# Kernel optimization log

Measured on AMD Instinct MI355X. Metric: run time of the kernel, lower is better.

Reference implementation:

```python
import jax, jax.numpy as jnp
import numpy as np
from jax import lax

GROUPS = 32
EPS = 1e-5
N_STEPS = 8   # fixed-step stand-in for adaptive implicit_adams
N_CORR = 2    # trapezoidal (Adams-Moulton) corrector iterations


def group_norm(x, gamma, beta):
    B, C, H, W = x.shape
    xg = x.reshape(B, GROUPS, C // GROUPS, H, W)
    mean = xg.mean(axis=(2, 3, 4), keepdims=True)
    var = xg.var(axis=(2, 3, 4), keepdims=True)
    xg = (xg - mean) * lax.rsqrt(var + EPS)
    return xg.reshape(B, C, H, W) * gamma[None, :, None, None] + beta[None, :, None, None]


def batch_norm1d(x, gamma, beta):  # training-mode batch stats, x: [B,C,L]
    mean = x.mean(axis=(0, 2), keepdims=True)
    var = x.var(axis=(0, 2), keepdims=True)
    return (x - mean) * lax.rsqrt(var + EPS) * gamma[None, :, None] + beta[None, :, None]


def conv1d(x, w, b):  # x [B,Cin,L], w [Cout,Cin,3], pad=1
    y = lax.conv_general_dilated(x, w, (1,), [(1, 1)], dimension_numbers=('NCH', 'OIH', 'NCH'))
    return y + b[None, :, None]


def concat_conv2d(t, x, w, b):  # x [B,C,H,W], w [C, C+1, 3,3], pad=1
    tt = jnp.full_like(x[:, :1], t)
    ttx = jnp.concatenate([tt, x], axis=1)
    y = lax.conv_general_dilated(ttx, w, (1, 1), [(1, 1), (1, 1)], dimension_numbers=('NCHW', 'OIHW', 'NCHW'))
    return y + b[None, :, None, None]


def make_odefunc(cw1, cb1, gn1_g, gn1_b, gn2_g, gn2_b, cw2, cb2, gn3_g, gn3_b):
    def f(t, x):
        out = jax.nn.relu(group_norm(x, gn1_g, gn1_b))
        out = concat_conv2d(t, out, cw1, cb1)
        out = jax.nn.elu(group_norm(out, gn2_g, gn2_b))
        out = concat_conv2d(t, out, cw2, cb2)
        return group_norm(out, gn3_g, gn3_b)
    return f


def ode_integrate(f, y0):
    h = 1.0 / N_STEPS

    def step(y, i):
        t = i.astype(y.dtype) * h
        f0 = f(t, y)
        y1 = y + h * f0  # explicit predictor
        for _ in range(N_CORR):  # implicit (trapezoidal AM) corrector
            y1 = y + 0.5 * h * (f0 + f(t + h, y1))
        return y1, None

    yT, _ = lax.scan(step, y0, jnp.arange(N_STEPS))
    return yT


def setup_inputs() -> dict:
    key = jax.random.key(0)
    ks = jax.random.split(key, 8)
    B, L, C = 16, 4096, 256
    inp = {
        'x': jax.random.normal(ks[0], (B, 4, 1, L), dtype=jnp.float32),
        'w1': jax.random.normal(ks[1], (64, 4, 3), dtype=jnp.float32) * 0.1,
        'b1': jnp.zeros((64,), jnp.float32),
        'bn1_g': jnp.ones((64,), jnp.float32), 'bn1_b': jnp.zeros((64,), jnp.float32),
        'w2': jax.random.normal(ks[2], (256, 64, 3), dtype=jnp.float32) * 0.05,
        'b2': jnp.zeros((256,), jnp.float32),
        'bn2_g': jnp.ones((256,), jnp.float32), 'bn2_b': jnp.zeros((256,), jnp.float32),
        'cw1': jax.random.normal(ks[3], (C, C + 1, 3, 3), dtype=jnp.float32) * 0.02,
        'cb1': jnp.zeros((C,), jnp.float32),
        'gn1_g': jnp.ones((C,), jnp.float32), 'gn1_b': jnp.zeros((C,), jnp.float32),
        'gn2_g': jnp.ones((C,), jnp.float32), 'gn2_b': jnp.zeros((C,), jnp.float32),
        'cw2': jax.random.normal(ks[4], (C, C + 1, 3, 3), dtype=jnp.float32) * 0.02,
        'cb2': jnp.zeros((C,), jnp.float32),
        'gn3_g': jnp.ones((C,), jnp.float32), 'gn3_b': jnp.zeros((C,), jnp.float32),
    }
    return inp


def reference(x, w1, b1, bn1_g, bn1_b, w2, b2, bn2_g, bn2_b,
              cw1, cb1, gn1_g, gn1_b, gn2_g, gn2_b, cw2, cb2, gn3_g, gn3_b):
    h = x[:, :, 0, :]                       # squeeze(2) -> [B,4,L]
    h = jax.nn.relu(batch_norm1d(conv1d(h, w1, b1), bn1_g, bn1_b))
    h = jnp.tanh(batch_norm1d(conv1d(h, w2, b2), bn2_g, bn2_b))
    y0 = h[:, :, None, :]                   # unsqueeze(2) -> [B,256,1,L]
    f = make_odefunc(cw1, cb1, gn1_g, gn1_b, gn2_g, gn2_b, cw2, cb2, gn3_g, gn3_b)
    return ode_integrate(f, y0)
```

## Files before the change

### kernel.cpp

```cpp
#include <hip/hip_runtime.h>
#include <math.h>

#define L4 4096

typedef short bf16x8 __attribute__((ext_vector_type(8)));
typedef float f32x4 __attribute__((ext_vector_type(4)));

__device__ __forceinline__ unsigned short f2bf(float f) {
  unsigned u = __builtin_bit_cast(unsigned, f);
  return (unsigned short)((u + 0x7FFFu + ((u >> 16) & 1u)) >> 16);
}
__device__ __forceinline__ float bf2f(unsigned short h) {
  unsigned u = ((unsigned)h) << 16;
  return __builtin_bit_cast(float, u);
}
__device__ __forceinline__ unsigned pk2(float lo, float hi) {
  unsigned d;
  asm("v_cvt_pk_bf16_f32 %0, %1, %2" : "=v"(d) : "v"(lo), "v"(hi));
  return d;
}
__device__ __forceinline__ float fast_tanh(float x) {
  float e = __expf(2.f * x);
  return 1.f - 2.f * __builtin_amdgcn_rcpf(e + 1.f);
}

__global__ __launch_bounds__(256) void pack_big(const float* __restrict__ cw,
                                                unsigned short* __restrict__ Apack,
                                                float* __restrict__ Tpack) {
  int gid = blockIdx.x * 256 + threadIdx.x;
  if (gid < 768) {
    int o = gid & 255, tap = gid >> 8;
    Tpack[tap * 256 + o] = cw[((size_t)o * 257) * 9 + 3 + tap];
  }
  if (gid >= 24 * 16 * 64) return;
  int ks = gid >> 10;
  int frow = (gid >> 6) & 15;
  int lane = gid & 63;
  int o = frow * 16 + (lane & 15);
  int tap = ks >> 3;
  int ib = ((ks & 7) << 5) + ((lane >> 4) << 3);
#pragma unroll
  for (int e = 0; e < 8; e++) {
    int i = ib + e;
    Apack[(size_t)gid * 8 + e] = f2bf(cw[((size_t)o * 257 + (i + 1)) * 9 + 3 + tap]);
  }
}

__global__ __launch_bounds__(256) void pack_stem(const float* __restrict__ w2,
                                                 unsigned short* __restrict__ Apack) {
  int gid = blockIdx.x * 256 + threadIdx.x;
  if (gid >= 6 * 16 * 64) return;
  int ks = gid >> 10;
  int frow = (gid >> 6) & 15;
  int lane = gid & 63;
  int o = frow * 16 + (lane & 15);
  int tap = ks >> 1;
  int ib = ((ks & 1) << 5) + ((lane >> 4) << 3);
#pragma unroll
  for (int e = 0; e < 8; e++) {
    int i = ib + e;
    Apack[(size_t)gid * 8 + e] = f2bf(w2[((size_t)o * 64 + i) * 3 + tap]);
  }
}

__global__ __launch_bounds__(256) void conv1_kernel(const float* __restrict__ x,
                                                    const float* __restrict__ w,
                                                    const float* __restrict__ bias,
                                                    unsigned short* __restrict__ out) {
  int idx = blockIdx.x * 256 + threadIdx.x;
  int l = idx & 4095;
  int c = (idx >> 12) & 63;
  int b = idx >> 18;
  const float* xb = x + (size_t)b * 4 * L4;
  const float* wc = w + c * 12;
  float acc = bias[c];
#pragma unroll
  for (int i = 0; i < 4; i++) {
    float x0 = (l > 0) ? xb[i * L4 + l - 1] : 0.f;
    float x1 = xb[i * L4 + l];
    float x2 = (l < 4095) ? xb[i * L4 + l + 1] : 0.f;
    acc += wc[i * 3] * x0 + wc[i * 3 + 1] * x1 + wc[i * 3 + 2] * x2;
  }
  out[idx] = f2bf(acc);
}

__global__ __launch_bounds__(256) void stats_kernel(const float* __restrict__ in,
                                                    float* __restrict__ stats,
                                                    int unit_stride, int nrow,
                                                    int row_stride, int rowlen,
                                                    float inv_n) {
  int u = blockIdx.x;
  const float* base = in + (size_t)u * unit_stride;
  float s = 0.f, s2 = 0.f;
  for (int r = 0; r < nrow; r++) {
    const float* rowp = base + (size_t)r * row_stride;
    for (int j = threadIdx.x * 4; j < rowlen; j += 256 * 4) {
      float4 v = *(const float4*)(rowp + j);
      s += v.x + v.y + v.z + v.w;
      s2 += v.x * v.x + v.y * v.y + v.z * v.z + v.w * v.w;
    }
  }
  __shared__ float sh[512];
  sh[threadIdx.x] = s;
  sh[256 + threadIdx.x] = s2;
  __syncthreads();
  for (int off = 128; off > 0; off >>= 1) {
    if (threadIdx.x < off) {
      sh[threadIdx.x] += sh[threadIdx.x + off];
      sh[256 + threadIdx.x] += sh[256 + threadIdx.x + off];
    }
    __syncthreads();
  }
  if (threadIdx.x == 0) {
    float m = sh[0] * inv_n;
    float var = sh[256] * inv_n - m * m;
    stats[u * 2] = m;
    stats[u * 2 + 1] = rsqrtf(var + 1e-5f);
  }
}

__global__ __launch_bounds__(256) void stats_bf16_kernel(const unsigned short* __restrict__ in,
                                                         float* __restrict__ stats,
                                                         int unit_stride, int nrow,
                                                         int row_stride, int rowlen,
                                                         float inv_n) {
  int u = blockIdx.x;
  const unsigned short* base = in + (size_t)u * unit_stride;
  float s = 0.f, s2 = 0.f;
  for (int r = 0; r < nrow; r++) {
    const unsigned short* rowp = base + (size_t)r * row_stride;
    for (int j = threadIdx.x * 4; j < rowlen; j += 256 * 4) {
      ushort4 v = *(const ushort4*)(rowp + j);
      float va = bf2f(v.x), vb = bf2f(v.y), vc = bf2f(v.z), vd = bf2f(v.w);
      s += va + vb + vc + vd;
      s2 += va * va + vb * vb + vc * vc + vd * vd;
    }
  }
  __shared__ float sh[512];
  sh[threadIdx.x] = s;
  sh[256 + threadIdx.x] = s2;
  __syncthreads();
  for (int off = 128; off > 0; off >>= 1) {
    if (threadIdx.x < off) {
      sh[threadIdx.x] += sh[threadIdx.x + off];
      sh[256 + threadIdx.x] += sh[256 + threadIdx.x + off];
    }
    __syncthreads();
  }
  if (threadIdx.x == 0) {
    float m = sh[0] * inv_n;
    float var = sh[256] * inv_n - m * m;
    stats[u * 2] = m;
    stats[u * 2 + 1] = rsqrtf(var + 1e-5f);
  }
}

__global__ __launch_bounds__(256) void act_transpose64(const unsigned short* __restrict__ inv,
                                                       const float* __restrict__ stats,
                                                       const float* __restrict__ gamma,
                                                       const float* __restrict__ beta,
                                                       unsigned short* __restrict__ Xt) {
  constexpr int C = 64;
  __shared__ unsigned short tile[64 * C];
  int bidx = blockIdx.x;
  int b = bidx >> 6;
  int lt = bidx & 63;
  int l0 = lt << 6;
  int t = threadIdx.x;
  int lanel = t & 63;
  int cq = t >> 6;
  for (int cp = 0; cp < C / 4; cp++) {
    int c = cp * 4 + cq;
    float m = stats[2 * c], rs = stats[2 * c + 1];
    float ga = gamma[c] * rs, be = beta[c] - m * ga;
    size_t gidx = ((size_t)b * C + c) * 4096 + l0 + lanel;
    float v = bf2f(inv[gidx]);
    float a = v * ga + be;
    float r = fmaxf(a, 0.f);
    int sw = (lanel & 15) << 2;
    tile[lanel * C + (c ^ sw)] = f2bf(r);
  }
  __syncthreads();
  constexpr int CH = C / 4;
  constexpr int RPP = 256 / CH;
  for (int p = 0; p < 64 / RPP; p++) {
    int r = p * RPP + t / CH;
    int ch = t % CH;
    int sw = (r & 15) << 2;
    ushort4 v = *(const ushort4*)&tile[r * C + ((ch * 4) ^ sw)];
    *(ushort4*)&Xt[((size_t)b * 4098 + 1 + l0 + r) * C + ch * 4] = v;
  }
  if (lt == 0) {
    if (t < C / 4) *(ushort4*)&Xt[((size_t)b * 4098 + 0) * C + t * 4] = make_ushort4(0, 0, 0, 0);
  } else if (lt == 63) {
    if (t < C / 4) *(ushort4*)&Xt[((size_t)b * 4098 + 4097) * C + t * 4] = make_ushort4(0, 0, 0, 0);
  }
}

template <int NKS, int KLG, int CIN, int NORM, int ACT, int NCH, bool INBF, bool TCH, int OUT>
__global__ __launch_bounds__(512, 4) void gemm_T(const void* __restrict__ Bsrc,
                                                 const unsigned short* __restrict__ Apack,
                                                 const float* __restrict__ Pin,
                                                 const float* __restrict__ gng,
                                                 const float* __restrict__ gnb,
                                                 const float* __restrict__ Tpack,
                                                 const float* __restrict__ bias,
                                                 float tval,
                                                 void* __restrict__ outv,
                                                 float* __restrict__ Pout) {
  constexpr int CPR = CIN / 8;
  constexpr int CPRLG = (CIN == 256) ? 5 : 3;
  constexpr int ROWS = 66;
  constexpr int RPI = 512 >> CPRLG;
  constexpr int TOT = ROWS * CPR;
  __shared__ unsigned short bsm[ROWS * CIN];
  __shared__ float gsm[32][2];
  __shared__ float ebias[256];
  __shared__ float psh[32][2];

  int tid = threadIdx.x;
  int lane = tid & 63;
  int wv = tid >> 6;
  int b = blockIdx.x >> 6;
  int lt = blockIdx.x & 63;
  int l_base = lt << 6;
  int wo0 = wv << 5;
  int col = lane & 15;
  int grp = lane >> 4;

  if (NORM) {
    int g = tid >> 4, j0 = tid & 15;
    const float* Pg = Pin + ((size_t)b * 32 + g) * 128;
    float s = 0.f, s2 = 0.f;
    for (int j = j0; j < NCH; j += 16) { s += Pg[j * 2]; s2 += Pg[j * 2 + 1]; }
#pragma unroll
    for (int off = 8; off; off >>= 1) { s += __shfl_down(s, off, 16); s2 += __shfl_down(s2, off, 16); }
    if (j0 == 0) {
      float m = s * (1.f / 32768.f);
      float var = s2 * (1.f / 32768.f) - m * m;
      gsm[g][0] = m;
      gsm[g][1] = rsqrtf(var + 1e-5f);
    }
  }
  if (tid < 256) {
    float e = bias[tid];
    if (TCH) e += tval * (Tpack[tid] + Tpack[256 + tid] + Tpack[512 + tid]);
    ebias[tid] = e;
  }
  if (OUT == 0 && tid >= 256 && tid < 288) { psh[tid - 256][0] = 0.f; psh[tid - 256][1] = 0.f; }
  __syncthreads();

  {
    int pl = tid & (CPR - 1);
    int row0 = tid >> CPRLG;
    int gch = pl ^ (row0 & 7);
    float ga0 = 1.f, ga1 = 1.f, ga2 = 1.f, ga3 = 1.f, ga4 = 1.f, ga5 = 1.f, ga6 = 1.f, ga7 = 1.f;
    float be0 = 0.f, be1 = 0.f, be2 = 0.f, be3 = 0.f, be4 = 0.f, be5 = 0.f, be6 = 0.f, be7 = 0.f;
    if (NORM) {
      float m = gsm[gch][0], rs = gsm[gch][1];
      float4 g0 = *(const float4*)&gng[gch * 8];
      float4 g1 = *(const float4*)&gng[gch * 8 + 4];
      float4 b0 = *(const float4*)&gnb[gch * 8];
      float4 b1 = *(const float4*)&gnb[gch * 8 + 4];
      ga0 = g0.x * rs; ga1 = g0.y * rs; ga2 = g0.z * rs; ga3 = g0.w * rs;
      ga4 = g1.x * rs; ga5 = g1.y * rs; ga6 = g1.z * rs; ga7 = g1.w * rs;
      be0 = b0.x - m * ga0; be1 = b0.y - m * ga1; be2 = b0.z - m * ga2; be3 = b0.w - m * ga3;
      be4 = b1.x - m * ga4; be5 = b1.y - m * ga5; be6 = b1.z - m * ga6; be7 = b1.w - m * ga7;
    }
#define ACTF(a) ((ACT == 0) ? fmaxf((a), 0.f) : ((a) > 0.f ? (a) : __expf(a) - 1.f))
#pragma unroll
    for (int it = 0; it < (TOT + 511) / 512; it++) {
      int chunk = it * 512 + tid;
      if (chunk < TOT) {
        int row = row0 + it * RPI;
        uint4 w4;
        if (NORM) {
          int gl = l_base - 1 + row;
          if (gl >= 0 && gl < 4096) {
            size_t base = ((size_t)b * 4096 + gl) * CIN + gch * 8;
            float v0, v1, v2, v3, v4, v5, v6, v7;
            if (INBF) {
              uint4 raw = *(const uint4*)((const unsigned short*)Bsrc + base);
              v0 = bf2f((unsigned short)(raw.x & 0xFFFF)); v1 = bf2f((unsigned short)(raw.x >> 16));
              v2 = bf2f((unsigned short)(raw.y & 0xFFFF)); v3 = bf2f((unsigned short)(raw.y >> 16));
              v4 = bf2f((unsigned short)(raw.z & 0xFFFF)); v5 = bf2f((unsigned short)(raw.z >> 16));
              v6 = bf2f((unsigned short)(raw.w & 0xFFFF)); v7 = bf2f((unsigned short)(raw.w >> 16));
            } else {
              float4 r0 = *(const float4*)((const float*)Bsrc + base);
              float4 r1 = *(const float4*)((const float*)Bsrc + base + 4);
              v0 = r0.x; v1 = r0.y; v2 = r0.z; v3 = r0.w;
              v4 = r1.x; v5 = r1.y; v6 = r1.z; v7 = r1.w;
            }
            float r0 = ACTF(v0 * ga0 + be0), r1 = ACTF(v1 * ga1 + be1);
            float r2 = ACTF(v2 * ga2 + be2), r3 = ACTF(v3 * ga3 + be3);
            float r4 = ACTF(v4 * ga4 + be4), r5 = ACTF(v5 * ga5 + be5);
            float r6 = ACTF(v6 * ga6 + be6), r7 = ACTF(v7 * ga7 + be7);
            w4.x = pk2(r0, r1); w4.y = pk2(r2, r3);
            w4.z = pk2(r4, r5); w4.w = pk2(r6, r7);
          } else {
            w4 = make_uint4(0, 0, 0, 0);
          }
        } else {
          w4 = *(const uint4*)((const unsigned short*)Bsrc +
                               ((size_t)b * 4098 + l_base + row) * CIN + gch * 8);
        }
        *(uint4*)&bsm[(size_t)chunk * 8] = w4;
      }
    }
#undef ACTF
  }
  __syncthreads();

  const unsigned short* apk = Apack + (size_t)(wv * 2) * 512 + (size_t)lane * 8;

  f32x4 acc[2][4];
#pragma unroll
  for (int i = 0; i < 2; i++)
#pragma unroll
    for (int j = 0; j < 4; j++) acc[i][j] = (f32x4){0.f, 0.f, 0.f, 0.f};

  __builtin_amdgcn_s_setprio(1);
  bf16x8 a00 = *(const bf16x8*)(apk);
  bf16x8 a01 = *(const bf16x8*)(apk + 512);
  bf16x8 a10 = *(const bf16x8*)(apk + 8192);
  bf16x8 a11 = *(const bf16x8*)(apk + 8192 + 512);
#pragma unroll
  for (int ksp = 0; ksp < NKS; ksp += 2) {
    bf16x8 n00, n01, n10, n11;
    constexpr bool dummy = false; (void)dummy;
    bool more = (ksp + 2) < NKS;
    if (more) {
      const unsigned short* apN0 = apk + (size_t)(ksp + 2) * 8192;
      const unsigned short* apN1 = apk + (size_t)(ksp + 3) * 8192;
      n00 = *(const bf16x8*)(apN0);
      n01 = *(const bf16x8*)(apN0 + 512);
      n10 = *(const bf16x8*)(apN1);
      n11 = *(const bf16x8*)(apN1 + 512);
    }
    {
      int ks = ksp;
      int tap = ks >> KLG;
      int cbase = (ks & ((1 << KLG) - 1)) << 2;
      int lr0 = col + tap;
      int cb = (cbase + grp) ^ (lr0 & 7);
      const unsigned short* bp = &bsm[((size_t)(lr0 << CPRLG) + cb) * 8];
      bf16x8 bfr[4];
#pragma unroll
      for (int fc = 0; fc < 4; fc++) bfr[fc] = *(const bf16x8*)(bp + fc * 16 * CIN);
#pragma unroll
      for (int fc = 0; fc < 4; fc++) {
        acc[0][fc] = __builtin_amdgcn_mfma_f32_16x16x32_bf16(a00, bfr[fc], acc[0][fc], 0, 0, 0);
        acc[1][fc] = __builtin_amdgcn_mfma_f32_16x16x32_bf16(a01, bfr[fc], acc[1][fc], 0, 0, 0);
      }
    }
    {
      int ks = ksp + 1;
      int tap = ks >> KLG;
      int cbase = (ks & ((1 << KLG) - 1)) << 2;
      int lr0 = col + tap;
      int cb = (cbase + grp) ^ (lr0 & 7);
      const unsigned short* bp = &bsm[((size_t)(lr0 << CPRLG) + cb) * 8];
      bf16x8 bfr[4];
#pragma unroll
      for (int fc = 0; fc < 4; fc++) bfr[fc] = *(const bf16x8*)(bp + fc * 16 * CIN);
#pragma unroll
      for (int fc = 0; fc < 4; fc++) {
        acc[0][fc] = __builtin_amdgcn_mfma_f32_16x16x32_bf16(a10, bfr[fc], acc[0][fc], 0, 0, 0);
        acc[1][fc] = __builtin_amdgcn_mfma_f32_16x16x32_bf16(a11, bfr[fc], acc[1][fc], 0, 0, 0);
      }
    }
    if (more) { a00 = n00; a01 = n01; a10 = n10; a11 = n11; }
  }
  __builtin_amdgcn_s_setprio(0);

  float ps = 0.f, ps2 = 0.f;
#pragma unroll
  for (int fo = 0; fo < 2; fo++) {
    int o0 = wo0 + fo * 16 + grp * 4;
    float eb0 = ebias[o0], eb1 = ebias[o0 + 1], eb2 = ebias[o0 + 2], eb3 = ebias[o0 + 3];
    float w0c0 = 0.f, w0c1 = 0.f, w0c2 = 0.f, w0c3 = 0.f;
    float w2c0 = 0.f, w2c1 = 0.f, w2c2 = 0.f, w2c3 = 0.f;
    if (TCH && lt == 0) {
      w0c0 = tval * Tpack[o0]; w0c1 = tval * Tpack[o0 + 1];
      w0c2 = tval * Tpack[o0 + 2]; w0c3 = tval * Tpack[o0 + 3];
    }
    if (TCH && lt == 63) {
      w2c0 = tval * Tpack[512 + o0]; w2c1 = tval * Tpack[512 + o0 + 1];
      w2c2 = tval * Tpack[512 + o0 + 2]; w2c3 = tval * Tpack[512 + o0 + 3];
    }
#pragma unroll
    for (int fc = 0; fc < 4; fc++) {
      int l = l_base + fc * 16 + col;
      float v0 = acc[fo][fc][0] + eb0;
      float v1 = acc[fo][fc][1] + eb1;
      float v2 = acc[fo][fc][2] + eb2;
      float v3 = acc[fo][fc][3] + eb3;
      if (TCH) {
        if (lt == 0 && l == 0) { v0 -= w0c0; v1 -= w0c1; v2 -= w0c2; v3 -= w0c3; }
        if (lt == 63 && l == 4095) { v0 -= w2c0; v1 -= w2c1; v2 -= w2c2; v3 -= w2c3; }
      }
      if (OUT == 0) {
        ps += v0 + v1 + v2 + v3;
        ps2 += v0 * v0 + v1 * v1 + v2 * v2 + v3 * v3;
        uint2 pk = make_uint2(pk2(v0, v1), pk2(v2, v3));
        *(uint2*)((unsigned short*)outv + ((size_t)b * 4096 + l) * 256 + o0) = pk;
      } else {
        float* op = (float*)outv + ((size_t)b * 256 + o0) * 4096 + l;
        op[0] = v0; op[4096] = v1; op[8192] = v2; op[12288] = v3;
      }
    }
    if (OUT == 0) {
      float s = ps, s2 = ps2;
#pragma unroll
      for (int off = 8; off; off >>= 1) {
        s += __shfl_down(s, off, 16);
        s2 += __shfl_down(s2, off, 16);
      }
      if (col == 0) {
        int g = wv * 4 + fo * 2 + (grp >> 1);
        atomicAdd(&psh[g][0], s);
        atomicAdd(&psh[g][1], s2);
      }
      ps = 0.f; ps2 = 0.f;
    }
  }

  if (OUT == 0) {
    __syncthreads();
    if (tid < 32) {
      size_t pi = ((size_t)b * 32 + tid) * 128 + (size_t)lt * 2;
      Pout[pi] = psh[tid][0];
      Pout[pi + 1] = psh[tid][1];
    }
  }
}

__global__ __launch_bounds__(512) void bn_tanh_T(const float* __restrict__ Q,
                                                 const float* __restrict__ stats,
                                                 const float* __restrict__ gamma,
                                                 const float* __restrict__ beta,
                                                 unsigned short* __restrict__ Y,
                                                 float* __restrict__ P1) {
  int tid = threadIdx.x;
  int b = blockIdx.x >> 5;
  int seg = blockIdx.x & 31;
  int c = tid >> 1;
  float m = stats[2 * c], rs = stats[2 * c + 1];
  float ga = gamma[c] * rs, be = beta[c] - m * ga;
  __shared__ float psh[32][2];
  if (tid < 32) { psh[tid][0] = 0.f; psh[tid][1] = 0.f; }
  __syncthreads();
  float s = 0.f, s2 = 0.f;
  for (int it = 0; it < 16; it++) {
    int l4 = (tid & 1) + it * 2;
    int l0 = seg * 128 + l4 * 4;
    float4 v = *(const float4*)&Q[((size_t)b * 256 + c) * 4096 + l0];
    float r0 = fast_tanh(v.x * ga + be);
    float r1 = fast_tanh(v.y * ga + be);
    float r2 = fast_tanh(v.z * ga + be);
    float r3 = fast_tanh(v.w * ga + be);
    Y[((size_t)b * 4096 + l0 + 0) * 256 + c] = f2bf(r0);
    Y[((size_t)b * 4096 + l0 + 1) * 256 + c] = f2bf(r1);
    Y[((size_t)b * 4096 + l0 + 2) * 256 + c] = f2bf(r2);
    Y[((size_t)b * 4096 + l0 + 3) * 256 + c] = f2bf(r3);
    s += r0 + r1 + r2 + r3;
    s2 += r0 * r0 + r1 * r1 + r2 * r2 + r3 * r3;
  }
#pragma unroll
  for (int off = 8; off; off >>= 1) { s += __shfl_down(s, off, 16); s2 += __shfl_down(s2, off, 16); }
  if ((tid & 15) == 0) {
    int g = c >> 3;
    atomicAdd(&psh[g][0], s);
    atomicAdd(&psh[g][1], s2);
  }
  __syncthreads();
  if (tid < 32) {
    size_t pi = ((size_t)b * 32 + tid) * 128 + (size_t)seg * 2;
    P1[pi] = psh[tid][0];
    P1[pi + 1] = psh[tid][1];
  }
}

template <int MODE>
__global__ __launch_bounds__(512) void combine_T(const unsigned short* __restrict__ F,
                                                 const float* __restrict__ P3,
                                                 const float* __restrict__ gng,
                                                 const float* __restrict__ gnb,
                                                 const unsigned short* __restrict__ Yin,
                                                 unsigned short* __restrict__ Out1,
                                                 unsigned short* __restrict__ OutB,
                                                 float* __restrict__ P1) {
  __shared__ float gsm[32][2];
  __shared__ float gabe[256][2];
  __shared__ float psh[32][2];
  int tid = threadIdx.x;
  int b = blockIdx.x >> 5;
  int seg = blockIdx.x & 31;
  {
    int g = tid >> 4, j0 = tid & 15;
    const float* Pg = P3 + ((size_t)b * 32 + g) * 128;
    float s = 0.f, s2 = 0.f;
    for (int j = j0; j < 64; j += 16) { s += Pg[j * 2]; s2 += Pg[j * 2 + 1]; }
#pragma unroll
    for (int off = 8; off; off >>= 1) { s += __shfl_down(s, off, 16); s2 += __shfl_down(s2, off, 16); }
    if (j0 == 0) {
      float m = s * (1.f / 32768.f);
      float var = s2 * (1.f / 32768.f) - m * m;
      gsm[g][0] = m;
      gsm[g][1] = rsqrtf(var + 1e-5f);
    }
  }
  __syncthreads();
  if (tid < 256) {
    float m = gsm[tid >> 3][0], rs = gsm[tid >> 3][1];
    float ga = gng[tid] * rs;
    gabe[tid][0] = ga;
    gabe[tid][1] = gnb[tid] - m * ga;
  }
  if (tid >= 256 && tid < 288) { psh[tid - 256][0] = 0.f; psh[tid - 256][1] = 0.f; }
  __syncthreads();

  size_t base4 = ((size_t)b * 4096 + seg * 128) * 64;
  int c0 = (tid << 2) & 255;
  int g = c0 >> 3;
  float ga0 = gabe[c0][0], be0 = gabe[c0][1];
  float ga1 = gabe[c0 + 1][0], be1 = gabe[c0 + 1][1];
  float ga2 = gabe[c0 + 2][0], be2 = gabe[c0 + 2][1];
  float ga3 = gabe[c0 + 3][0], be3 = gabe[c0 + 3][1];
  float s = 0.f, s2 = 0.f;
  for (int i = tid; i < 8192; i += 512) {
    size_t idx4 = base4 + i;
    ushort4 fv = ((const ushort4*)F)[idx4];
    ushort4 yv = ((const ushort4*)Yin)[idx4];
    float y0 = bf2f(yv.x), y1v = bf2f(yv.y), y2 = bf2f(yv.z), y3 = bf2f(yv.w);
    float f0 = bf2f(fv.x) * ga0 + be0;
    float f1 = bf2f(fv.y) * ga1 + be1;
    float f2 = bf2f(fv.z) * ga2 + be2;
    float f3 = bf2f(fv.w) * ga3 + be3;
    float yn0 = y0 + (MODE == 0 ? 0.125f : 0.0625f) * f0;
    float yn1 = y1v + (MODE == 0 ? 0.125f : 0.0625f) * f1;
    float yn2 = y2 + (MODE == 0 ? 0.125f : 0.0625f) * f2;
    float yn3 = y3 + (MODE == 0 ? 0.125f : 0.0625f) * f3;
    ((uint2*)Out1)[idx4] = make_uint2(pk2(yn0, yn1), pk2(yn2, yn3));
    if (MODE == 0) {
      float yb0 = y0 + 0.0625f * f0;
      float yb1 = y1v + 0.0625f * f1;
      float yb2 = y2 + 0.0625f * f2;
      float yb3 = y3 + 0.0625f * f3;
      ((uint2*)OutB)[idx4] = make_uint2(pk2(yb0, yb1), pk2(yb2, yb3));
    }
    s += yn0 + yn1 + yn2 + yn3;
    s2 += yn0 * yn0 + yn1 * yn1 + yn2 * yn2 + yn3 * yn3;
  }
  s += __shfl_xor(s, 1);
  s2 += __shfl_xor(s2, 1);
  if ((tid & 1) == 0) {
    atomicAdd(&psh[g][0], s);
    atomicAdd(&psh[g][1], s2);
  }
  __syncthreads();
  if (tid < 32) {
    size_t pi = ((size_t)b * 32 + tid) * 128 + (size_t)seg * 2;
    P1[pi] = psh[tid][0];
    P1[pi + 1] = psh[tid][1];
  }
}

__global__ __launch_bounds__(256) void transpose_final(const unsigned short* __restrict__ Y,
                                                       float* __restrict__ out) {
  __shared__ unsigned short tile[64 * 260];
  int b = blockIdx.x >> 6;
  int lt = blockIdx.x & 63;
  int t = threadIdx.x;
  for (int i = t; i < 4096; i += 256) {
    int r = i >> 6;
    int c4 = (i & 63) << 2;
    ushort4 v = *(const ushort4*)&Y[((size_t)b * 4096 + lt * 64 + r) * 256 + c4];
    *(ushort4*)&tile[r * 260 + c4] = v;
  }
  __syncthreads();
  for (int i = t; i < 4096; i += 256) {
    int c = i >> 4;
    int l4 = (i & 15) << 2;
    float4 v;
    v.x = bf2f(tile[(l4 + 0) * 260 + c]);
    v.y = bf2f(tile[(l4 + 1) * 260 + c]);
    v.z = bf2f(tile[(l4 + 2) * 260 + c]);
    v.w = bf2f(tile[(l4 + 3) * 260 + c]);
    *(float4*)&out[((size_t)b * 256 + c) * 4096 + lt * 64 + l4] = v;
  }
}

extern "C" void kernel_launch(void* const* d_in, const int* in_sizes, int n_in,
                              void* d_out, int out_size, void* d_ws, size_t ws_size,
                              hipStream_t stream) {
  const float* x = (const float*)d_in[0];
  const float* w1 = (const float*)d_in[1];
  const float* b1 = (const float*)d_in[2];
  const float* bn1_g = (const float*)d_in[3];
  const float* bn1_b = (const float*)d_in[4];
  const float* w2 = (const float*)d_in[5];
  const float* b2 = (const float*)d_in[6];
  const float* bn2_g = (const float*)d_in[7];
  const float* bn2_b = (const float*)d_in[8];
  const float* cw1 = (const float*)d_in[9];
  const float* cb1 = (const float*)d_in[10];
  const float* gn1_g = (const float*)d_in[11];
  const float* gn1_b = (const float*)d_in[12];
  const float* gn2_g = (const float*)d_in[13];
  const float* gn2_b = (const float*)d_in[14];
  const float* cw2 = (const float*)d_in[15];
  const float* cb2 = (const float*)d_in[16];
  const float* gn3_g = (const float*)d_in[17];
  const float* gn3_b = (const float*)d_in[18];

  const size_t SZ = (size_t)16 * 256 * 4096;

  char* p = (char*)d_ws;
  unsigned short* Ybf = (unsigned short*)p;  p += SZ * 2;
  unsigned short* C1 = (unsigned short*)p;   p += SZ * 2;
  unsigned short* Fb = (unsigned short*)p;   p += SZ * 2;
  unsigned short* APK1 = (unsigned short*)p; p += (size_t)24 * 16 * 64 * 8 * 2;
  unsigned short* APK2 = (unsigned short*)p; p += (size_t)24 * 16 * 64 * 8 * 2;
  unsigned short* APKS = (unsigned short*)p; p += (size_t)6 * 16 * 64 * 8 * 2;
  float* TP1 = (float*)p;                    p += 768 * 4;
  float* TP2 = (float*)p;                    p += 768 * 4;
  float* STATS = (float*)p;                  p += 1024 * 4;
  float* P1 = (float*)p;                     p += (size_t)16 * 32 * 128 * 4;
  float* P2 = (float*)p;                     p += (size_t)16 * 32 * 128 * 4;
  float* P3 = (float*)p;                     p += (size_t)16 * 32 * 128 * 4;

  float* Q = (float*)d_out;
  unsigned short* Y1 = (unsigned short*)d_out;
  unsigned short* YB = Y1 + SZ;

  pack_big<<<96, 256, 0, stream>>>(cw1, APK1, TP1);
  pack_big<<<96, 256, 0, stream>>>(cw2, APK2, TP2);
  pack_stem<<<24, 256, 0, stream>>>(w2, APKS);

  conv1_kernel<<<16384, 256, 0, stream>>>(x, w1, b1, C1);
  stats_bf16_kernel<<<64, 256, 0, stream>>>(C1, STATS, 4096, 16, 64 * 4096, 4096, 1.f / 65536.f);
  act_transpose64<<<1024, 256, 0, stream>>>(C1, STATS, bn1_g, bn1_b, Fb);
  gemm_T<6, 1, 64, 0, 0, 32, true, false, 1><<<1024, 512, 0, stream>>>(
      Fb, APKS, nullptr, nullptr, nullptr, nullptr, b2, 0.f, Q, nullptr);
  stats_kernel<<<256, 256, 0, stream>>>(Q, STATS, 4096, 16, 256 * 4096, 4096, 1.f / 65536.f);
  bn_tanh_T<<<512, 512, 0, stream>>>(Q, STATS, bn2_g, bn2_b, Ybf, P1);

  const float H = 0.125f;
  for (int i = 0; i < 8; i++) {
    float t = i * H;
    gemm_T<24, 3, 256, 1, 0, 32, true, true, 0><<<1024, 512, 0, stream>>>(
        Ybf, APK1, P1, gn1_g, gn1_b, TP1, cb1, t, C1, P2);
    gemm_T<24, 3, 256, 1, 1, 64, true, true, 0><<<1024, 512, 0, stream>>>(
        C1, APK2, P2, gn2_g, gn2_b, TP2, cb2, t, Fb, P3);
    combine_T<0><<<512, 512, 0, stream>>>(Fb, P3, gn3_g, gn3_b, Ybf, Y1, YB, P1);
    for (int c = 0; c < 2; c++) {
      gemm_T<24, 3, 256, 1, 0, 32, true, true, 0><<<1024, 512, 0, stream>>>(
          Y1, APK1, P1, gn1_g, gn1_b, TP1, cb1, t + H, C1, P2);
      gemm_T<24, 3, 256, 1, 1, 64, true, true, 0><<<1024, 512, 0, stream>>>(
          C1, APK2, P2, gn2_g, gn2_b, TP2, cb2, t + H, Fb, P3);
      if (c == 0)
        combine_T<1><<<512, 512, 0, stream>>>(Fb, P3, gn3_g, gn3_b, YB, Y1, nullptr, P1);
      else
        combine_T<2><<<512, 512, 0, stream>>>(Fb, P3, gn3_g, gn3_b, YB, Ybf, nullptr, P1);
    }
  }

  transpose_final<<<1024, 256, 0, stream>>>(Ybf, (float*)d_out);
}
```

Baseline: 2.420 ms.

## Prefetch gemm input tiles to registers, simplify MFMA loop, store stem output as bf16

```diff
diff --git a/kernel.cpp b/kernel.cpp
--- a/kernel.cpp
+++ b/kernel.cpp
@@ -82,41 +82,6 @@
     acc += wc[i * 3] * x0 + wc[i * 3 + 1] * x1 + wc[i * 3 + 2] * x2;
   }
   out[idx] = f2bf(acc);
-}
-
-__global__ __launch_bounds__(256) void stats_kernel(const float* __restrict__ in,
-                                                    float* __restrict__ stats,
-                                                    int unit_stride, int nrow,
-                                                    int row_stride, int rowlen,
-                                                    float inv_n) {
-  int u = blockIdx.x;
-  const float* base = in + (size_t)u * unit_stride;
-  float s = 0.f, s2 = 0.f;
-  for (int r = 0; r < nrow; r++) {
-    const float* rowp = base + (size_t)r * row_stride;
-    for (int j = threadIdx.x * 4; j < rowlen; j += 256 * 4) {
-      float4 v = *(const float4*)(rowp + j);
-      s += v.x + v.y + v.z + v.w;
-      s2 += v.x * v.x + v.y * v.y + v.z * v.z + v.w * v.w;
-    }
-  }
-  __shared__ float sh[512];
-  sh[threadIdx.x] = s;
-  sh[256 + threadIdx.x] = s2;
-  __syncthreads();
-  for (int off = 128; off > 0; off >>= 1) {
-    if (threadIdx.x < off) {
-      sh[threadIdx.x] += sh[threadIdx.x + off];
-      sh[256 + threadIdx.x] += sh[256 + threadIdx.x + off];
-    }
-    __syncthreads();
-  }
-  if (threadIdx.x == 0) {
-    float m = sh[0] * inv_n;
-    float var = sh[256] * inv_n - m * m;
-    stats[u * 2] = m;
-    stats[u * 2 + 1] = rsqrtf(var + 1e-5f);
-  }
 }
 
 __global__ __launch_bounds__(256) void stats_bf16_kernel(const unsigned short* __restrict__ in,
@@ -213,6 +178,7 @@
   constexpr int ROWS = 66;
   constexpr int RPI = 512 >> CPRLG;
   constexpr int TOT = ROWS * CPR;
+  constexpr int NIT = (TOT + 511) / 512;
   __shared__ unsigned short bsm[ROWS * CIN];
   __shared__ float gsm[32][2];
   __shared__ float ebias[256];
@@ -228,6 +194,36 @@
   int col = lane & 15;
   int grp = lane >> 4;
 
+  int pl = tid & (CPR - 1);
+  int row0s = tid >> CPRLG;
+  int gch = pl ^ (row0s & 7);
+  uint4 hA[NIT];
+  uint4 hB[NIT];
+#pragma unroll
+  for (int it = 0; it < NIT; it++) {
+    hA[it] = make_uint4(0, 0, 0, 0);
+    if (NORM && !INBF) hB[it] = make_uint4(0, 0, 0, 0);
+    int chunk = it * 512 + tid;
+    if (chunk < TOT) {
+      int row = row0s + it * RPI;
+      if (NORM) {
+        int gl = l_base - 1 + row;
+        if (gl >= 0 && gl < 4096) {
+          size_t base = ((size_t)b * 4096 + gl) * CIN + gch * 8;
+          if (INBF) {
+            hA[it] = *(const uint4*)((const unsigned short*)Bsrc + base);
+          } else {
+            hA[it] = *(const uint4*)((const float*)Bsrc + base);
+            hB[it] = *(const uint4*)((const float*)Bsrc + base + 4);
+          }
+        }
+      } else {
+        hA[it] = *(const uint4*)((const unsigned short*)Bsrc +
+                                 ((size_t)b * 4098 + l_base + row) * CIN + gch * 8);
+      }
+    }
+  }
+
   if (NORM) {
     int g = tid >> 4, j0 = tid & 15;
     const float* Pg = Pin + ((size_t)b * 32 + g) * 128;
@@ -251,9 +247,6 @@
   __syncthreads();
 
   {
-    int pl = tid & (CPR - 1);
-    int row0 = tid >> CPRLG;
-    int gch = pl ^ (row0 & 7);
     float ga0 = 1.f, ga1 = 1.f, ga2 = 1.f, ga3 = 1.f, ga4 = 1.f, ga5 = 1.f, ga6 = 1.f, ga7 = 1.f;
     float be0 = 0.f, be1 = 0.f, be2 = 0.f, be3 = 0.f, be4 = 0.f, be5 = 0.f, be6 = 0.f, be7 = 0.f;
     if (NORM) {
@@ -269,27 +262,29 @@
     }
 #define ACTF(a) ((ACT == 0) ? fmaxf((a), 0.f) : ((a) > 0.f ? (a) : __expf(a) - 1.f))
 #pragma unroll
-    for (int it = 0; it < (TOT + 511) / 512; it++) {
+    for (int it = 0; it < NIT; it++) {
       int chunk = it * 512 + tid;
       if (chunk < TOT) {
-        int row = row0 + it * RPI;
+        int row = row0s + it * RPI;
         uint4 w4;
         if (NORM) {
           int gl = l_base - 1 + row;
           if (gl >= 0 && gl < 4096) {
-            size_t base = ((size_t)b * 4096 + gl) * CIN + gch * 8;
             float v0, v1, v2, v3, v4, v5, v6, v7;
             if (INBF) {
-              uint4 raw = *(const uint4*)((const unsigned short*)Bsrc + base);
-              v0 = bf2f((unsigned short)(raw.x & 0xFFFF)); v1 = bf2f((unsigned short)(raw.x >> 16));
-              v2 = bf2f((unsigned short)(raw.y & 0xFFFF)); v3 = bf2f((unsigned short)(raw.y >> 16));
-              v4 = bf2f((unsigned short)(raw.z & 0xFFFF)); v5 = bf2f((unsigned short)(raw.z >> 16));
-              v6 = bf2f((unsigned short)(raw.w & 0xFFFF)); v7 = bf2f((unsigned short)(raw.w >> 16));
+              v0 = bf2f((unsigned short)(hA[it].x & 0xFFFF)); v1 = bf2f((unsigned short)(hA[it].x >> 16));
+              v2 = bf2f((unsigned short)(hA[it].y & 0xFFFF)); v3 = bf2f((unsigned short)(hA[it].y >> 16));
+              v4 = bf2f((unsigned short)(hA[it].z & 0xFFFF)); v5 = bf2f((unsigned short)(hA[it].z >> 16));
+              v6 = bf2f((unsigned short)(hA[it].w & 0xFFFF)); v7 = bf2f((unsigned short)(hA[it].w >> 16));
             } else {
-              float4 r0 = *(const float4*)((const float*)Bsrc + base);
-              float4 r1 = *(const float4*)((const float*)Bsrc + base + 4);
-              v0 = r0.x; v1 = r0.y; v2 = r0.z; v3 = r0.w;
-              v4 = r1.x; v5 = r1.y; v6 = r1.z; v7 = r1.w;
+              v0 = __builtin_bit_cast(float, hA[it].x);
+              v1 = __builtin_bit_cast(float, hA[it].y);
+              v2 = __builtin_bit_cast(float, hA[it].z);
+              v3 = __builtin_bit_cast(float, hA[it].w);
+              v4 = __builtin_bit_cast(float, hB[it].x);
+              v5 = __builtin_bit_cast(float, hB[it].y);
+              v6 = __builtin_bit_cast(float, hB[it].z);
+              v7 = __builtin_bit_cast(float, hB[it].w);
             }
             float r0 = ACTF(v0 * ga0 + be0), r1 = ACTF(v1 * ga1 + be1);
             float r2 = ACTF(v2 * ga2 + be2), r3 = ACTF(v3 * ga3 + be3);
@@ -301,8 +296,7 @@
             w4 = make_uint4(0, 0, 0, 0);
           }
         } else {
-          w4 = *(const uint4*)((const unsigned short*)Bsrc +
-                               ((size_t)b * 4098 + l_base + row) * CIN + gch * 8);
+          w4 = hA[it];
         }
         *(uint4*)&bsm[(size_t)chunk * 8] = w4;
       }
@@ -320,56 +314,24 @@
     for (int j = 0; j < 4; j++) acc[i][j] = (f32x4){0.f, 0.f, 0.f, 0.f};
 
   __builtin_amdgcn_s_setprio(1);
-  bf16x8 a00 = *(const bf16x8*)(apk);
-  bf16x8 a01 = *(const bf16x8*)(apk + 512);
-  bf16x8 a10 = *(const bf16x8*)(apk + 8192);
-  bf16x8 a11 = *(const bf16x8*)(apk + 8192 + 512);
-#pragma unroll
-  for (int ksp = 0; ksp < NKS; ksp += 2) {
-    bf16x8 n00, n01, n10, n11;
-    constexpr bool dummy = false; (void)dummy;
-    bool more = (ksp + 2) < NKS;
-    if (more) {
-      const unsigned short* apN0 = apk + (size_t)(ksp + 2) * 8192;
-      const unsigned short* apN1 = apk + (size_t)(ksp + 3) * 8192;
-      n00 = *(const bf16x8*)(apN0);
-      n01 = *(const bf16x8*)(apN0 + 512);
-      n10 = *(const bf16x8*)(apN1);
-      n11 = *(const bf16x8*)(apN1 + 512);
-    }
-    {
-      int ks = ksp;
-      int tap = ks >> KLG;
-      int cbase = (ks & ((1 << KLG) - 1)) << 2;
-      int lr0 = col + tap;
-      int cb = (cbase + grp) ^ (lr0 & 7);
-      const unsigned short* bp = &bsm[((size_t)(lr0 << CPRLG) + cb) * 8];
-      bf16x8 bfr[4];
-#pragma unroll
-      for (int fc = 0; fc < 4; fc++) bfr[fc] = *(const bf16x8*)(bp + fc * 16 * CIN);
-#pragma unroll
-      for (int fc = 0; fc < 4; fc++) {
-        acc[0][fc] = __builtin_amdgcn_mfma_f32_16x16x32_bf16(a00, bfr[fc], acc[0][fc], 0, 0, 0);
-        acc[1][fc] = __builtin_amdgcn_mfma_f32_16x16x32_bf16(a01, bfr[fc], acc[1][fc], 0, 0, 0);
-      }
-    }
-    {
-      int ks = ksp + 1;
-      int tap = ks >> KLG;
-      int cbase = (ks & ((1 << KLG) - 1)) << 2;
-      int lr0 = col + tap;
-      int cb = (cbase + grp) ^ (lr0 & 7);
-      const unsigned short* bp = &bsm[((size_t)(lr0 << CPRLG) + cb) * 8];
-      bf16x8 bfr[4];
-#pragma unroll
-      for (int fc = 0; fc < 4; fc++) bfr[fc] = *(const bf16x8*)(bp + fc * 16 * CIN);
-#pragma unroll
-      for (int fc = 0; fc < 4; fc++) {
-        acc[0][fc] = __builtin_amdgcn_mfma_f32_16x16x32_bf16(a10, bfr[fc], acc[0][fc], 0, 0, 0);
-        acc[1][fc] = __builtin_amdgcn_mfma_f32_16x16x32_bf16(a11, bfr[fc], acc[1][fc], 0, 0, 0);
-      }
-    }
-    if (more) { a00 = n00; a01 = n01; a10 = n10; a11 = n11; }
+#pragma unroll
+  for (int ks = 0; ks < NKS; ks++) {
+    int tap = ks >> KLG;
+    int cbase = (ks & ((1 << KLG) - 1)) << 2;
+    int lr0 = col + tap;
+    int cb = (cbase + grp) ^ (lr0 & 7);
+    const unsigned short* bp = &bsm[((size_t)(lr0 << CPRLG) + cb) * 8];
+    const unsigned short* ap = apk + (size_t)ks * 16 * 512;
+    bf16x8 bfr[4], afr[2];
+#pragma unroll
+    for (int fc = 0; fc < 4; fc++) bfr[fc] = *(const bf16x8*)(bp + fc * 16 * CIN);
+#pragma unroll
+    for (int fo = 0; fo < 2; fo++) afr[fo] = *(const bf16x8*)(ap + fo * 512);
+#pragma unroll
+    for (int fo = 0; fo < 2; fo++)
+#pragma unroll
+      for (int fc = 0; fc < 4; fc++)
+        acc[fo][fc] = __builtin_amdgcn_mfma_f32_16x16x32_bf16(afr[fo], bfr[fc], acc[fo][fc], 0, 0, 0);
   }
   __builtin_amdgcn_s_setprio(0);
 
@@ -404,9 +366,12 @@
         ps2 += v0 * v0 + v1 * v1 + v2 * v2 + v3 * v3;
         uint2 pk = make_uint2(pk2(v0, v1), pk2(v2, v3));
         *(uint2*)((unsigned short*)outv + ((size_t)b * 4096 + l) * 256 + o0) = pk;
-      } else {
+      } else if (OUT == 1) {
         float* op = (float*)outv + ((size_t)b * 256 + o0) * 4096 + l;
         op[0] = v0; op[4096] = v1; op[8192] = v2; op[12288] = v3;
+      } else {
+        unsigned short* op = (unsigned short*)outv + ((size_t)b * 256 + o0) * 4096 + l;
+        op[0] = f2bf(v0); op[4096] = f2bf(v1); op[8192] = f2bf(v2); op[12288] = f2bf(v3);
       }
     }
     if (OUT == 0) {
@@ -435,7 +400,7 @@
   }
 }
 
-__global__ __launch_bounds__(512) void bn_tanh_T(const float* __restrict__ Q,
+__global__ __launch_bounds__(512) void bn_tanh_T(const unsigned short* __restrict__ Q,
                                                  const float* __restrict__ stats,
                                                  const float* __restrict__ gamma,
                                                  const float* __restrict__ beta,
@@ -454,11 +419,11 @@
   for (int it = 0; it < 16; it++) {
     int l4 = (tid & 1) + it * 2;
     int l0 = seg * 128 + l4 * 4;
-    float4 v = *(const float4*)&Q[((size_t)b * 256 + c) * 4096 + l0];
-    float r0 = fast_tanh(v.x * ga + be);
-    float r1 = fast_tanh(v.y * ga + be);
-    float r2 = fast_tanh(v.z * ga + be);
-    float r3 = fast_tanh(v.w * ga + be);
+    ushort4 v = *(const ushort4*)&Q[((size_t)b * 256 + c) * 4096 + l0];
+    float r0 = fast_tanh(bf2f(v.x) * ga + be);
+    float r1 = fast_tanh(bf2f(v.y) * ga + be);
+    float r2 = fast_tanh(bf2f(v.z) * ga + be);
+    float r3 = fast_tanh(bf2f(v.w) * ga + be);
     Y[((size_t)b * 4096 + l0 + 0) * 256 + c] = f2bf(r0);
     Y[((size_t)b * 4096 + l0 + 1) * 256 + c] = f2bf(r1);
     Y[((size_t)b * 4096 + l0 + 2) * 256 + c] = f2bf(r2);
@@ -630,7 +595,7 @@
   float* P2 = (float*)p;                     p += (size_t)16 * 32 * 128 * 4;
   float* P3 = (float*)p;                     p += (size_t)16 * 32 * 128 * 4;
 
-  float* Q = (float*)d_out;
+  unsigned short* Qbf = (unsigned short*)d_out;
   unsigned short* Y1 = (unsigned short*)d_out;
   unsigned short* YB = Y1 + SZ;
 
@@ -641,10 +606,10 @@
   conv1_kernel<<<16384, 256, 0, stream>>>(x, w1, b1, C1);
   stats_bf16_kernel<<<64, 256, 0, stream>>>(C1, STATS, 4096, 16, 64 * 4096, 4096, 1.f / 65536.f);
   act_transpose64<<<1024, 256, 0, stream>>>(C1, STATS, bn1_g, bn1_b, Fb);
-  gemm_T<6, 1, 64, 0, 0, 32, true, false, 1><<<1024, 512, 0, stream>>>(
-      Fb, APKS, nullptr, nullptr, nullptr, nullptr, b2, 0.f, Q, nullptr);
-  stats_kernel<<<256, 256, 0, stream>>>(Q, STATS, 4096, 16, 256 * 4096, 4096, 1.f / 65536.f);
-  bn_tanh_T<<<512, 512, 0, stream>>>(Q, STATS, bn2_g, bn2_b, Ybf, P1);
+  gemm_T<6, 1, 64, 0, 0, 32, true, false, 2><<<1024, 512, 0, stream>>>(
+      Fb, APKS, nullptr, nullptr, nullptr, nullptr, b2, 0.f, Qbf, nullptr);
+  stats_bf16_kernel<<<256, 256, 0, stream>>>(Qbf, STATS, 4096, 16, 256 * 4096, 4096, 1.f / 65536.f);
+  bn_tanh_T<<<512, 512, 0, stream>>>(Qbf, STATS, bn2_g, bn2_b, Ybf, P1);
 
   const float H = 0.125f;
   for (int i = 0; i < 8; i++) {
```

Measured after the change: 2.452 ms. Within noise of the previous version (+1.3%).
